# Optimization experiments

Hardware: AMD Instinct MI355X
Metric: run time of the kernel (lower is better)

The kernel has to match this reference:

```python
import jax, jax.numpy as jnp
import numpy as np

B, C, H, W = 4, 16, 512, 512

# 8-connectivity offsets in the exact order the torch double loop visits them
_OFFSETS = [(-1, -1), (-1, 0), (-1, 1), (0, -1), (0, 1), (1, -1), (1, 0), (1, 1)]


def _make_edge_index(height, width):
    """Vectorized grid_8 edge index, matching torch's per-node-then-offset order."""
    n = height * width
    dst = np.zeros((n, 8), dtype=np.int64)
    mask = np.zeros((n, 8), dtype=bool)
    hh = np.arange(height)[:, None]
    ww = np.arange(width)[None, :]
    for k, (dh, dw) in enumerate(_OFFSETS):
        nh, nw = hh + dh, ww + dw
        valid = (nh >= 0) & (nh < height) & (nw >= 0) & (nw < width)
        nb = np.clip(nh, 0, height - 1) * width + np.clip(nw, 0, width - 1)
        dst[:, k] = nb.reshape(-1)
        mask[:, k] = valid.reshape(-1)
    src = np.repeat(np.arange(n, dtype=np.int64), 8).reshape(n, 8)
    m = mask.reshape(-1)
    return np.stack([src.reshape(-1)[m], dst.reshape(-1)[m]], axis=0)  # [2, E]


def setup_inputs() -> dict:
    key = jax.random.key(0)
    grid_features = jax.random.normal(key, (B, C, H, W), dtype=jnp.float32)
    edge_index = jnp.asarray(_make_edge_index(H, W))  # [2, 2091012]
    return {"grid_features": grid_features, "edge_index": edge_index}


def reference(grid_features, edge_index):
    b, c, h, w = grid_features.shape
    # (B, C, H, W) -> (B*H*W, C) node features
    grid_flat = jnp.transpose(grid_features, (0, 2, 3, 1)).reshape(b, h * w, c)
    node_features = grid_flat.reshape(b * h * w, c)

    src, dst = edge_index[0], edge_index[1]
    src_h, src_w = src // w, src % w
    dst_h, dst_w = dst // w, dst % w
    spatial_dist = jnp.sqrt(
        (src_h - dst_h).astype(jnp.float32) ** 2
        + (src_w - dst_w).astype(jnp.float32) ** 2
    )  # [E]

    # per-edge |src - dst| feature diff, mean over channels, then mean over batch
    diff = jnp.abs(grid_flat[:, src, :] - grid_flat[:, dst, :]).mean(axis=-1)  # [B, E]
    feature_diff = diff.mean(axis=0)  # [E]

    edge_attr = jnp.stack([spatial_dist, feature_diff], axis=1)  # [E, 2]
    return node_features, edge_index, edge_attr
```

## Files before the change

kernel.cpp:

```cpp
#include <hip/hip_runtime.h>

#define HW  (512 * 512)
#define NC  16
#define NB  4
#define GW  512
#define GH  512
#define TILE 16
#define HALO 18
#define NSU  12

__device__ __forceinline__ unsigned int bfr(float f) {
    union { float f; unsigned int u; } v; v.f = f;
    return (v.u + 0x7fffu + ((v.u >> 16) & 1u)) >> 16;
}
__device__ __forceinline__ float blo(unsigned int u) {
    union { unsigned int u; float f; } v; v.u = u << 16; return v.f;
}
__device__ __forceinline__ float bhi(unsigned int u) {
    union { unsigned int u; float f; } v; v.u = u & 0xffff0000u; return v.f;
}

__device__ __forceinline__ int edge_prefix(int h, int w) {
    if (h == 0) return (w == 0) ? 0 : 3 + 5 * (w - 1);
    int p = 2556 + 4090 * (h - 1);
    if (h == GH - 1) return p + ((w == 0) ? 0 : 3 + 5 * (w - 1));
    return p + ((w == 0) ? 0 : 5 + 8 * (w - 1));
}
__device__ __forceinline__ int degree(int h, int w) {
    int rh = 1 + (h > 0) + (h < GH - 1);
    int rw = 1 + (w > 0) + (w < GW - 1);
    return rh * rw - 1;
}

__global__ __launch_bounds__(256) void k_fused(const float* __restrict__ g,
                                               float* __restrict__ nf_out,
                                               float* __restrict__ ei_out,
                                               float* __restrict__ attr_out,
                                               int E) {
    __shared__ unsigned int nds[HALO * HALO * NSU];
    float* fdbuf = (float*)nds;

    const int tid = threadIdx.x;
    const int bx = blockIdx.x & 31, by = blockIdx.x >> 5;
    const int h0 = by * TILE, w0 = bx * TILE;
    const int tr = tid >> 4, tc = tid & 15;

    const int OFF_H[8] = {-1, -1, -1, 0, 0, 1, 1, 1};
    const int OFF_W[8] = {-1, 0, 1, -1, 1, -1, 0, 1};

    float acc[8];
#pragma unroll
    for (int k = 0; k < 8; ++k) acc[k] = 0.0f;

    for (int b = 0; b < NB; ++b) {
        __syncthreads();

        for (int r = 0; r < 4; ++r) {
            int idx = r * 256 + tid;
            if (idx < 864) {
                int f4  = idx % 6;
                int t   = idx / 6;
                int row = t % 18;
                int c2  = t / 18;
                int hh  = min(max(h0 - 1 + row, 0), GH - 1);
                int gw  = min(max(w0 - 4 + 4 * f4, 0), GW - 4);
                const float* pA = g + (((size_t)(b * 16 + 2 * c2)) << 18) + (hh << 9) + gw;
                const float4 A = *(const float4*)pA;
                const float4 B = *(const float4*)(pA + HW);
#pragma unroll
                for (int j = 0; j < 4; ++j) {
                    int hc = 4 * f4 + j - 3;
                    if ((unsigned)hc < (unsigned)HALO) {
                        float a  = ((const float*)&A)[j];
                        float bb = ((const float*)&B)[j];
                        nds[(row * HALO + hc) * NSU + c2] = bfr(a) | (bfr(bb) << 16);
                    }
                }
            }
        }
        __syncthreads();

#pragma unroll
        for (int s = 0; s < 4; ++s) {
            int o4 = s * 256 + tid;
            int c4 = o4 & 3;
            int nl256 = o4 >> 2;
            int pr = nl256 >> 4, pc = nl256 & 15;
            int nl = (pr + 1) * HALO + (pc + 1);
            unsigned int u0 = nds[nl * NSU + 2 * c4];
            unsigned int u1 = nds[nl * NSU + 2 * c4 + 1];
            int n = (h0 + pr) * GW + (w0 + pc);
            float4* dst = (float4*)(nf_out + (((size_t)b << 18) + n) * NC + 4 * c4);
            *dst = make_float4(blo(u0), bhi(u0), blo(u1), bhi(u1));
        }

        {
            const uint4* p = (const uint4*)nds;
            int nl_self = (tr + 1) * HALO + (tc + 1);
            uint4 s0 = p[nl_self * 3];
            uint4 s1 = p[nl_self * 3 + 1];
#pragma unroll
            for (int k = 0; k < 8; ++k) {
                int nl_n = (tr + 1 + OFF_H[k]) * HALO + (tc + 1 + OFF_W[k]);
                uint4 n0 = p[nl_n * 3];
                uint4 n1 = p[nl_n * 3 + 1];
                float a = 0.0f;
                a += fabsf(blo(s0.x) - blo(n0.x)) + fabsf(bhi(s0.x) - bhi(n0.x));
                a += fabsf(blo(s0.y) - blo(n0.y)) + fabsf(bhi(s0.y) - bhi(n0.y));
                a += fabsf(blo(s0.z) - blo(n0.z)) + fabsf(bhi(s0.z) - bhi(n0.z));
                a += fabsf(blo(s0.w) - blo(n0.w)) + fabsf(bhi(s0.w) - bhi(n0.w));
                a += fabsf(blo(s1.x) - blo(n1.x)) + fabsf(bhi(s1.x) - bhi(n1.x));
                a += fabsf(blo(s1.y) - blo(n1.y)) + fabsf(bhi(s1.y) - bhi(n1.y));
                a += fabsf(blo(s1.z) - blo(n1.z)) + fabsf(bhi(s1.z) - bhi(n1.z));
                a += fabsf(blo(s1.w) - blo(n1.w)) + fabsf(bhi(s1.w) - bhi(n1.w));
                acc[k] += a;
            }
        }
    }

    __syncthreads();

    {
        int h = h0 + tr, w = w0 + tc;
        int cnt = 0;
#pragma unroll
        for (int k = 0; k < 8; ++k) {
            if ((unsigned)(h + OFF_H[k]) < (unsigned)GH &&
                (unsigned)(w + OFF_W[k]) < (unsigned)GW) {
                fdbuf[tid * 9 + cnt] = acc[k] * (1.0f / 64.0f);
                ++cnt;
            }
        }
    }
    __syncthreads();

#pragma unroll
    for (int r = 0; r < 8; ++r) {
        int u2    = r * 256 + tid;
        int chunk = u2 >> 7;
        int e     = u2 & 127;
        int h     = h0 + chunk;
        int first = degree(h, w0);
        int mid   = degree(h, w0 + 1);
        int last  = degree(h, w0 + TILE - 1);
        int Lr    = first + 14 * mid + last;
        if (e < Lr) {
            int node_in_row, k;
            if (e < first) { node_in_row = 0; k = e; }
            else {
                int m = e - first;
                if (mid == 8) { node_in_row = 1 + (m >> 3); k = m & 7; }
                else          { int q = m / 5; node_in_row = 1 + q; k = m - 5 * q; }
            }
            int w = w0 + node_in_row;
            int n = h * GW + w;
            int idx = 0, cnt2 = 0;
#pragma unroll
            for (int i = 0; i < 8; ++i) {
                bool ok = (unsigned)(h + OFF_H[i]) < (unsigned)GH &&
                          (unsigned)(w + OFF_W[i]) < (unsigned)GW;
                if (ok) { if (cnt2 == k) idx = i; ++cnt2; }
            }
            int dh = OFF_H[idx], dw = OFF_W[idx];
            float dist = (dh != 0 && dw != 0) ? 1.41421356237f : 1.0f;
            float fd = fdbuf[(chunk * 16 + node_in_row) * 9 + k];
            int o = edge_prefix(h, w0) + e;
            ei_out[o]     = (float)n;
            ei_out[E + o] = (float)(n + dh * GW + dw);
            *(float2*)(attr_out + 2 * (size_t)o) = make_float2(dist, fd);
        }
    }
}

extern "C" void kernel_launch(void* const* d_in, const int* in_sizes, int n_in,
                              void* d_out, int out_size, void* d_ws, size_t ws_size,
                              hipStream_t stream) {
    const float* g = (const float*)d_in[0];
    int E = in_sizes[1] / 2;

    float* out      = (float*)d_out;
    float* nf_out   = out;
    float* ei_out   = out + (size_t)NB * HW * NC;
    float* attr_out = ei_out + (size_t)2 * E;

    k_fused<<<(GH / TILE) * (GW / TILE), 256, 0, stream>>>(g, nf_out, ei_out, attr_out, E);
}
```

Before: 187.1 us.

## Prefetch next batch tile into registers and swizzle block-to-tile mapping

Hoists the per-thread halo address and slot computation out of the batch loop and software-pipelines the global loads, so the next batch's float4 loads are issued right after the current batch's LDS write. Their latency then overlaps the node-feature stores and the neighbour diff compute. It also remaps blockIdx so consecutive blocks take tiles 128 apart, which spreads concurrent blocks across the image, and it adds a min-blocks-per-SM hint of 4 to launch_bounds. The cost is extra registers for the staged loads (LA/LB and the precomputed pointers), which could limit occupancy.

```diff
diff --git a/kernel.cpp b/kernel.cpp
--- a/kernel.cpp
+++ b/kernel.cpp
@@ -32,53 +32,80 @@
     return rh * rw - 1;
 }
 
-__global__ __launch_bounds__(256) void k_fused(const float* __restrict__ g,
-                                               float* __restrict__ nf_out,
-                                               float* __restrict__ ei_out,
-                                               float* __restrict__ attr_out,
-                                               int E) {
+#define STAGE_LOAD(b)                                                          \
+    do {                                                                       \
+        _Pragma("unroll") for (int r = 0; r < 4; ++r) if (vld[r]) {            \
+            const float* p = pb[r] + ((size_t)(b) << 22);                      \
+            LA[r] = *(const float4*)p;                                         \
+            LB[r] = *(const float4*)(p + HW);                                  \
+        }                                                                      \
+    } while (0)
+
+#define STAGE_WRITE()                                                          \
+    do {                                                                       \
+        _Pragma("unroll") for (int r = 0; r < 4; ++r) if (vld[r]) {            \
+            _Pragma("unroll") for (int j = 0; j < 4; ++j) {                    \
+                int hc = vhc[r] + j;                                           \
+                if ((unsigned)hc < (unsigned)HALO) {                           \
+                    float a  = ((const float*)&LA[r])[j];                      \
+                    float bb = ((const float*)&LB[r])[j];                      \
+                    nds[vslot[r] + j * NSU] = bfr(a) | (bfr(bb) << 16);        \
+                }                                                              \
+            }                                                                  \
+        }                                                                      \
+    } while (0)
+
+__global__ __launch_bounds__(256, 4) void k_fused(const float* __restrict__ g,
+                                                  float* __restrict__ nf_out,
+                                                  float* __restrict__ ei_out,
+                                                  float* __restrict__ attr_out,
+                                                  int E) {
     __shared__ unsigned int nds[HALO * HALO * NSU];
     float* fdbuf = (float*)nds;
 
     const int tid = threadIdx.x;
-    const int bx = blockIdx.x & 31, by = blockIdx.x >> 5;
+    const int til = ((blockIdx.x & 7) << 7) | (blockIdx.x >> 3);
+    const int bx = til & 31, by = til >> 5;
     const int h0 = by * TILE, w0 = bx * TILE;
     const int tr = tid >> 4, tc = tid & 15;
 
     const int OFF_H[8] = {-1, -1, -1, 0, 0, 1, 1, 1};
     const int OFF_W[8] = {-1, 0, 1, -1, 1, -1, 0, 1};
 
+    bool vld[4];
+    const float* pb[4];
+    int vslot[4], vhc[4];
+#pragma unroll
+    for (int r = 0; r < 4; ++r) {
+        int idx = r * 256 + tid;
+        vld[r] = idx < 864;
+        int i2  = vld[r] ? idx : 0;
+        int f4  = i2 % 6;
+        int t   = i2 / 6;
+        int row = t % 18;
+        int c2  = t / 18;
+        int hh  = min(max(h0 - 1 + row, 0), GH - 1);
+        int gw  = min(max(w0 - 4 + 4 * f4, 0), GW - 4);
+        pb[r]   = g + (((size_t)(2 * c2)) << 18) + (hh << 9) + gw;
+        vhc[r]  = 4 * f4 - 3;
+        vslot[r] = (row * HALO + 4 * f4 - 3) * NSU + c2;
+    }
+
     float acc[8];
 #pragma unroll
     for (int k = 0; k < 8; ++k) acc[k] = 0.0f;
 
+    float4 LA[4], LB[4];
+    STAGE_LOAD(0);
+
+#pragma unroll
     for (int b = 0; b < NB; ++b) {
         __syncthreads();
 
-        for (int r = 0; r < 4; ++r) {
-            int idx = r * 256 + tid;
-            if (idx < 864) {
-                int f4  = idx % 6;
-                int t   = idx / 6;
-                int row = t % 18;
-                int c2  = t / 18;
-                int hh  = min(max(h0 - 1 + row, 0), GH - 1);
-                int gw  = min(max(w0 - 4 + 4 * f4, 0), GW - 4);
-                const float* pA = g + (((size_t)(b * 16 + 2 * c2)) << 18) + (hh << 9) + gw;
-                const float4 A = *(const float4*)pA;
-                const float4 B = *(const float4*)(pA + HW);
-#pragma unroll
-                for (int j = 0; j < 4; ++j) {
-                    int hc = 4 * f4 + j - 3;
-                    if ((unsigned)hc < (unsigned)HALO) {
-                        float a  = ((const float*)&A)[j];
-                        float bb = ((const float*)&B)[j];
-                        nds[(row * HALO + hc) * NSU + c2] = bfr(a) | (bfr(bb) << 16);
-                    }
-                }
-            }
-        }
+        STAGE_WRITE();
         __syncthreads();
+
+        if (b + 1 < NB) STAGE_LOAD(b + 1);
 
 #pragma unroll
         for (int s = 0; s < 4; ++s) {
```

Measured after the change: 512.8 us. +174.2%, slower.
